# Performance work log

Hardware: AMD Instinct MI355X
Metric: run time of the kernel (lower is better)

## Reference

```python
import jax, jax.numpy as jnp
import numpy as np

B, T, D, HS = 8, 2048, 768, 64
H = D // HS  # 12 heads
LN_EPS = 1e-5


def setup_inputs() -> dict:
    key = jax.random.key(0)
    ks = jax.random.split(key, 8)
    s = 0.02
    x = jax.random.normal(ks[0], (B, T, D), jnp.float32)
    Wx = jax.random.normal(ks[1], (D, D), jnp.float32) * s
    Ww = jax.random.normal(ks[2], (D, D), jnp.float32) * 0.01  # w_proj.weight ~ N(0,0.01)
    # w_proj bias schedule: logit(1 - linspace(0.9,0.999,H)) per head, expanded over head_size
    r_sched = jnp.linspace(0.9, 0.999, H)
    w_target = 1.0 - r_sched
    bw = jnp.log(w_target / (1.0 - w_target))          # logit
    bw = jnp.repeat(bw[:, None], HS, axis=1).reshape(-1)  # (D,)
    Wk = jax.random.normal(ks[3], (D, D), jnp.float32) * s
    Wv = jax.random.normal(ks[4], (D, D), jnp.float32) * s
    Wr = jax.random.normal(ks[5], (D, D), jnp.float32) * s
    Wo = jax.random.normal(ks[6], (D, D), jnp.float32) * s
    gamma = jnp.ones((D,), jnp.float32)
    beta = jnp.zeros((D,), jnp.float32)
    return {"x": x, "Wx": Wx, "Ww": Ww, "bw": bw, "Wk": Wk, "Wv": Wv,
            "Wr": Wr, "Wo": Wo, "gamma": gamma, "beta": beta}


def _layernorm(x, gamma, beta):
    mu = jnp.mean(x, axis=-1, keepdims=True)
    var = jnp.mean(jnp.square(x - mu), axis=-1, keepdims=True)
    return (x - mu) * jax.lax.rsqrt(var + LN_EPS) * gamma + beta


def _selective_scan(k, v, w):
    """k,v,w: (T,B,H,HS). State S: (B,H,HS,HS).
    S_t = (1 - w_t) * S_{t-1} (decay along key dim) + k_t (x) v_t;  y_t = k_t . S_t."""
    S0 = jnp.zeros((B, H, HS, HS), k.dtype)

    def step(S, inp):
        kt, vt, wt = inp  # each (B,H,HS)
        S = S * (1.0 - wt)[..., :, None] + kt[..., :, None] * vt[..., None, :]
        yt = jnp.einsum('bhi,bhij->bhj', kt, S)
        return S, yt

    _, ys = jax.lax.scan(step, S0, (k, v, w))
    return ys  # (T,B,H,HS)


def reference(x, Wx, Ww, bw, Wk, Wv, Wr, Wo, gamma, beta):
    xn = _layernorm(x, gamma, beta)                       # (B,T,D)
    xp = jnp.einsum('btd,ed->bte', xn, Wx)                # x_proj
    w = jax.nn.sigmoid(jnp.einsum('bte,fe->btf', xp, Ww) + bw)
    k = jnp.einsum('btd,ed->bte', xn, Wk)
    v = jnp.einsum('btd,ed->bte', xn, Wv)
    r = jax.nn.sigmoid(jnp.einsum('btd,ed->bte', xn, Wr))

    def to_scan(a):  # (B,T,D) -> (T,B,H,HS)
        return a.reshape(B, T, H, HS).transpose(1, 0, 2, 3)

    ys = _selective_scan(to_scan(k), to_scan(v), to_scan(w))  # (T,B,H,HS)
    y = ys.transpose(1, 0, 2, 3).reshape(B, T, D)
    y = y * r
    return jnp.einsum('btd,ed->bte', y, Wo)
```

## Files before the change

kernel.cpp:

```cpp
#include <hip/hip_runtime.h>

#define B_ 8
#define T_ 2048
#define D_ 768
#define H_ 12
#define HS_ 64
#define LN_EPS 1e-5f
#define NC 32
#define TC 64

typedef __attribute__((ext_vector_type(8))) short bf16x8;
typedef __attribute__((ext_vector_type(4))) float f32x4;

__device__ __forceinline__ ushort f2bf(float f) {
  unsigned u = __builtin_bit_cast(unsigned, f);
  unsigned r = (u + 0x7FFFu + ((u >> 16) & 1u)) >> 16;
  return (ushort)r;
}
__device__ __forceinline__ float bf2f(ushort u) {
  return __builtin_bit_cast(float, ((unsigned)u) << 16);
}

__device__ __forceinline__ int fragaddr(int t, int i) {
  return ((t >> 4) * 2 + (i >> 5)) * 512 + ((((i >> 3) & 3) * 16) + (t & 15)) * 8 + (i & 7);
}
__device__ __forceinline__ int fragswz(int i) {
  return (((i >> 3) & 3) << 3) ^ (((i >> 5) & 1) << 5);
}

__global__ __launch_bounds__(256) void zero_out_kernel(float* __restrict__ out, int n) {
  for (int i = blockIdx.x * 256 + threadIdx.x; i < n; i += gridDim.x * 256)
    out[i] = 0.f;
}

__global__ __launch_bounds__(256) void cast5_kernel(
    const float* __restrict__ w0, const float* __restrict__ w1,
    const float* __restrict__ w2, const float* __restrict__ w3,
    const float* __restrict__ w4, ushort* __restrict__ dst) {
  const float* srcs[5] = {w0, w1, w2, w3, w4};
  const int slots[5] = {0, 1, 2, 4, 5};
  const float* src = srcs[blockIdx.y];
  ushort* d = dst + (size_t)slots[blockIdx.y] * 589824;
  int idx = (blockIdx.x * 256 + threadIdx.x) * 4;
  float4 v = *reinterpret_cast<const float4*>(src + idx);
  ushort4 o;
  o.x = f2bf(v.x); o.y = f2bf(v.y); o.z = f2bf(v.z); o.w = f2bf(v.w);
  *reinterpret_cast<ushort4*>(d + idx) = o;
}

__global__ __launch_bounds__(256) void transpose_cast_kernel(
    const float* __restrict__ src, ushort* __restrict__ dst) {
  __shared__ ushort tile[32][33];
  const int bx = blockIdx.x * 32;
  const int by = blockIdx.y * 32;
  const int tx = threadIdx.x & 31, ty = threadIdx.x >> 5;
#pragma unroll
  for (int r = 0; r < 32; r += 8)
    tile[ty + r][tx] = f2bf(src[(size_t)(by + ty + r) * 768 + bx + tx]);
  __syncthreads();
#pragma unroll
  for (int r = 0; r < 32; r += 8)
    dst[(size_t)(bx + ty + r) * 768 + by + tx] = tile[tx][ty + r];
}

__global__ __launch_bounds__(256) void ln_kernel(
    const float* __restrict__ x, const float* __restrict__ gamma,
    const float* __restrict__ beta, ushort* __restrict__ xn) {
  const int wv = threadIdx.x >> 6;
  const int lane = threadIdx.x & 63;
  const int row = blockIdx.x * 4 + wv;
  const float* xr = x + (size_t)row * D_;
  float4 a[3];
#pragma unroll
  for (int s = 0; s < 3; ++s)
    a[s] = *reinterpret_cast<const float4*>(xr + s * 256 + lane * 4);
  float sum = 0.f;
#pragma unroll
  for (int s = 0; s < 3; ++s) sum += a[s].x + a[s].y + a[s].z + a[s].w;
#pragma unroll
  for (int off = 32; off; off >>= 1) sum += __shfl_xor(sum, off);
  float mu = sum * (1.f / 768.f);
  float vs = 0.f;
#pragma unroll
  for (int s = 0; s < 3; ++s) {
    float dx = a[s].x - mu, dy = a[s].y - mu, dz = a[s].z - mu, dw = a[s].w - mu;
    vs += dx * dx + dy * dy + dz * dz + dw * dw;
  }
#pragma unroll
  for (int off = 32; off; off >>= 1) vs += __shfl_xor(vs, off);
  float rs = rsqrtf(vs * (1.f / 768.f) + LN_EPS);
  ushort* orow = xn + (size_t)row * D_;
#pragma unroll
  for (int s = 0; s < 3; ++s) {
    int col = s * 256 + lane * 4;
    float4 g = *reinterpret_cast<const float4*>(gamma + col);
    float4 bb = *reinterpret_cast<const float4*>(beta + col);
    ushort4 o;
    o.x = f2bf((a[s].x - mu) * rs * g.x + bb.x);
    o.y = f2bf((a[s].y - mu) * rs * g.y + bb.y);
    o.z = f2bf((a[s].z - mu) * rs * g.z + bb.z);
    o.w = f2bf((a[s].w - mu) * rs * g.w + bb.w);
    *reinterpret_cast<ushort4*>(orow + col) = o;
  }
}

__global__ __launch_bounds__(512, 2) void gemm256(
    const ushort* __restrict__ A, const ushort* __restrict__ W,
    float* __restrict__ Cf,
    ushort* __restrict__ d0, ushort* __restrict__ d1,
    ushort* __restrict__ d2, ushort* __restrict__ d3, int mode) {
  __shared__ __align__(16) ushort lds[65536];
  const int tid = threadIdx.x;
  const int wid = tid >> 6;
  const int lane = tid & 63;
  const int wr = wid >> 2, wc = wid & 3;
  const int fr = lane & 15, fq = lane >> 4;
  const int m0 = blockIdx.x * 256, n0 = blockIdx.y * 256;
  const int strow = tid >> 3;
  const int stblk = tid & 7;

  const int RA0 = wr * 8192;
  const int RA1 = 32768 + wr * 8192;
  const int RB0 = 16384 + (wc >> 1) * 8192 + (wc & 1) * 4096;
  const int RB1 = 49152 + (wc >> 1) * 8192 + (wc & 1) * 4096;

  f32x4 acc[8][4];
#pragma unroll
  for (int m = 0; m < 8; ++m)
#pragma unroll
    for (int n = 0; n < 4; ++n) acc[m][n] = (f32x4){0.f, 0.f, 0.f, 0.f};

#define STAGE_HALF(gb, grow0, kk0, roff)                                          \
  {                                                                               \
    _Pragma("unroll") for (int j = 0; j < 2; ++j) {                               \
      const int lr_ = j * 64 + strow;                                             \
      const int bs_ = stblk ^ (lr_ & 7);                                          \
      const ushort* s_ = (gb) + (size_t)((grow0) + lr_) * 768 + (kk0) + bs_ * 8;  \
      __builtin_amdgcn_global_load_lds(                                           \
          (const __attribute__((address_space(1))) void*)s_,                      \
          (__attribute__((address_space(3))) void*)(lds + (roff) + j * 4096 + wid * 512), \
          16, 0, 0);                                                              \
    }                                                                             \
  }

#define LDF(dst, base, rf, kk)                                                    \
  dst = *reinterpret_cast<const bf16x8*>(                                         \
      lds + (base) + ((rf)*16 + fr) * 64 + ((((kk)*4 + fq) ^ (fr & 7)) * 8));

#define MFMA_Q(mb, nb, aa, bb)                                                    \
  __builtin_amdgcn_s_setprio(1);                                                  \
  _Pragma("unroll") for (int m_ = 0; m_ < 4; ++m_)                                \
  _Pragma("unroll") for (int n_ = 0; n_ < 2; ++n_)                                \
  _Pragma("unroll") for (int k_ = 0; k_ < 2; ++k_)                                \
    acc[(mb) + m_][(nb) + n_] = __builtin_amdgcn_mfma_f32_16x16x32_bf16(          \
        aa[m_][k_], bb[n_][k_], acc[(mb) + m_][(nb) + n_], 0, 0, 0);              \
  __builtin_amdgcn_s_setprio(0);

  STAGE_HALF(A, m0, 0, 0);
  STAGE_HALF(A, m0 + 128, 0, 8192);
  STAGE_HALF(W, n0, 0, 16384);
  STAGE_HALF(W, n0 + 128, 0, 24576);
  STAGE_HALF(W, n0, 64, 49152);
  STAGE_HALF(W, n0 + 128, 64, 57344);
  asm volatile("s_waitcnt vmcnt(4)" ::: "memory");
  __builtin_amdgcn_s_barrier();

  bf16x8 aL[4][2], aH[4][2], bL[2][2], bH[2][2];

  for (int i = 0; i < 6; ++i) {
    const int kQ = (2 * i + 1) * 64;
    const int kP2 = (2 * i + 2 <= 11 ? 2 * i + 2 : 11) * 64;
    const int kQ2 = (2 * i + 3 <= 11 ? 2 * i + 3 : 11) * 64;

    STAGE_HALF(A, m0, kQ, 32768);
#pragma unroll
    for (int m = 0; m < 4; ++m) { LDF(aL[m][0], RA0, m, 0); LDF(aL[m][1], RA0, m, 1); }
#pragma unroll
    for (int n = 0; n < 2; ++n) { LDF(bL[n][0], RB0, n, 0); LDF(bL[n][1], RB0, n, 1); }
    __builtin_amdgcn_s_barrier();
    MFMA_Q(0, 0, aL, bL);
    __builtin_amdgcn_s_barrier();

    STAGE_HALF(A, m0 + 128, kQ, 40960);
#pragma unroll
    for (int n = 0; n < 2; ++n) { LDF(bH[n][0], RB0, n + 2, 0); LDF(bH[n][1], RB0, n + 2, 1); }
    __builtin_amdgcn_s_barrier();
    MFMA_Q(0, 2, aL, bH);
    __builtin_amdgcn_s_barrier();

    STAGE_HALF(W, n0, kP2, 16384);
#pragma unroll
    for (int m = 0; m < 4; ++m) { LDF(aH[m][0], RA0, m + 4, 0); LDF(aH[m][1], RA0, m + 4, 1); }
    __builtin_amdgcn_s_barrier();
    MFMA_Q(4, 0, aH, bL);
    __builtin_amdgcn_s_barrier();

    STAGE_HALF(W, n0 + 128, kP2, 24576);
    __builtin_amdgcn_s_barrier();
    MFMA_Q(4, 2, aH, bH);
    asm volatile("s_waitcnt vmcnt(4)" ::: "memory");
    __builtin_amdgcn_s_barrier();

    STAGE_HALF(A, m0, kP2, 0);
#pragma unroll
    for (int m = 0; m < 4; ++m) { LDF(aL[m][0], RA1, m, 0); LDF(aL[m][1], RA1, m, 1); }
#pragma unroll
    for (int n = 0; n < 2; ++n) { LDF(bL[n][0], RB1, n, 0); LDF(bL[n][1], RB1, n, 1); }
    __builtin_amdgcn_s_barrier();
    MFMA_Q(0, 0, aL, bL);
    __builtin_amdgcn_s_barrier();

    STAGE_HALF(A, m0 + 128, kP2, 8192);
#pragma unroll
    for (int n = 0; n < 2; ++n) { LDF(bH[n][0], RB1, n + 2, 0); LDF(bH[n][1], RB1, n + 2, 1); }
    __builtin_amdgcn_s_barrier();
    MFMA_Q(0, 2, aL, bH);
    __builtin_amdgcn_s_barrier();

    STAGE_HALF(W, n0, kQ2, 49152);
#pragma unroll
    for (int m = 0; m < 4; ++m) { LDF(aH[m][0], RA1, m + 4, 0); LDF(aH[m][1], RA1, m + 4, 1); }
    __builtin_amdgcn_s_barrier();
    MFMA_Q(4, 0, aH, bL);
    __builtin_amdgcn_s_barrier();

    STAGE_HALF(W, n0 + 128, kQ2, 57344);
    __builtin_amdgcn_s_barrier();
    MFMA_Q(4, 2, aH, bH);
    asm volatile("s_waitcnt vmcnt(4)" ::: "memory");
    __builtin_amdgcn_s_barrier();
  }

  const int r0 = fq * 4;
  if (mode == 5) {
    const int sel = n0 >= 2304 ? 3 : n0 >= 1536 ? 2 : n0 >= 768 ? 1 : 0;
    const int nb = n0 - sel * 768;
    if (sel == 1) {
#pragma unroll
      for (int mf = 0; mf < 8; ++mf)
#pragma unroll
        for (int nf = 0; nf < 4; ++nf) {
          int gr = m0 + wr * 128 + mf * 16 + r0;
          int gc = nb + wc * 64 + nf * 16 + fr;
          int b = gr >> 11, t = gr & 2047;
          int c = t >> 6, s0 = t & 63;
          int h = gc >> 6, j = gc & 63;
          size_t addr = ((size_t)((b * 12 + h) * 32 + c)) * 4096 +
                        (size_t)(((j >> 4) * 2 + (s0 >> 5)) * 512 +
                                 (((s0 >> 3) & 3) * 16 + (j & 15)) * 8 + (s0 & 7));
          ushort4 o;
          o.x = f2bf(acc[mf][nf][0]); o.y = f2bf(acc[mf][nf][1]);
          o.z = f2bf(acc[mf][nf][2]); o.w = f2bf(acc[mf][nf][3]);
          *reinterpret_cast<ushort4*>(d1 + addr) = o;
        }
    } else {
      ushort* dst = sel == 0 ? d0 : sel == 2 ? d2 : d3;
      const bool sig = (sel == 2);
#pragma unroll
      for (int mf = 0; mf < 8; ++mf)
#pragma unroll
        for (int nf = 0; nf < 4; ++nf) {
          int gr = m0 + wr * 128 + mf * 16 + r0;
          int gc = nb + wc * 64 + nf * 16 + fr;
#pragma unroll
          for (int rr = 0; rr < 4; ++rr) {
            float v = acc[mf][nf][rr];
            if (sig) v = 1.f / (1.f + __expf(-v));
            dst[(size_t)(gr + rr) * 768 + gc] = f2bf(v);
          }
        }
    }
  } else {
#pragma unroll
    for (int mf = 0; mf < 8; ++mf)
#pragma unroll
      for (int nf = 0; nf < 4; ++nf) {
        int gr = m0 + wr * 128 + mf * 16 + r0;
        int gc = n0 + wc * 64 + nf * 16 + fr;
#pragma unroll
        for (int rr = 0; rr < 4; ++rr)
          Cf[(size_t)(gr + rr) * 768 + gc] = acc[mf][nf][rr];
      }
  }
#undef STAGE_HALF
#undef LDF
#undef MFMA_Q
}

__global__ __launch_bounds__(256) void scan_mc3(
    const ushort* __restrict__ kb, const ushort* __restrict__ zb,
    const ushort* __restrict__ vbF, const float* __restrict__ bwp,
    ushort* __restrict__ McT, float* __restrict__ aend) {
  __shared__ ushort kt[64 * 72];
  __shared__ ushort zt[64 * 72];
  __shared__ ushort kIAfA[4096];
  __shared__ float part[256];
  const int bh = blockIdx.x, c = blockIdx.y;
  const int b = bh / H_, h = bh % H_;
  const int tid = threadIdx.x;
  const int w = tid >> 6, lane = tid & 63;
  const int fr = lane & 15, fq = lane >> 4;
  const int row = tid >> 2, c16 = (tid & 3) * 16;
  const float bwh = bwp[h * 64];

  {
    const ushort* gk = kb + ((size_t)(b * T_ + c * TC + row)) * 768 + h * 64 + c16;
    const ushort* gz = zb + ((size_t)(b * T_ + c * TC + row)) * 768 + h * 64 + c16;
    uint4 k0 = *(const uint4*)gk, k1 = *(const uint4*)(gk + 8);
    uint4 z0 = *(const uint4*)gz, z1 = *(const uint4*)(gz + 8);
    *reinterpret_cast<uint4*>(&kt[row * 72 + c16]) = k0;
    *reinterpret_cast<uint4*>(&kt[row * 72 + c16 + 8]) = k1;
    *reinterpret_cast<uint4*>(&zt[row * 72 + c16]) = z0;
    *reinterpret_cast<uint4*>(&zt[row * 72 + c16 + 8]) = z1;
  }
  bf16x8 vfr[8];
  {
    const ushort* vch = vbF + ((size_t)bh * NC + c) * 4096;
#pragma unroll
    for (int f = 0; f < 8; ++f)
      vfr[f] = *reinterpret_cast<const bf16x8*>(vch + f * 512 + lane * 8);
  }
  __syncthreads();
  float dreg[16];
  float p = 1.f;
#pragma unroll
  for (int tt = 0; tt < 16; ++tt) {
    float z = bf2f(zt[(w * 16 + tt) * 72 + lane]);
    float d = 1.f / (1.f + __expf(z + bwh));
    dreg[tt] = d;
    p *= d;
  }
  part[w * 64 + lane] = p;
  __syncthreads();
  float a = 1.f;
  for (int w2 = 0; w2 < w; ++w2) a *= part[w2 * 64 + lane];
  if (w == 0)
    aend[((size_t)bh * NC + c) * 64 + lane] =
        part[lane] * part[64 + lane] * part[128 + lane] * part[192 + lane];
#pragma unroll
  for (int tt = 0; tt < 16; ++tt) {
    int t = w * 16 + tt;
    float k = bf2f(kt[t * 72 + lane]);
    a *= dreg[tt];
    kIAfA[fragaddr(lane, t)] = f2bf(k / a);
  }
  __syncthreads();

  bf16x8 af2[2];
#pragma unroll
  for (int kk = 0; kk < 2; ++kk)
    af2[kk] = *reinterpret_cast<const bf16x8*>(&kIAfA[(w * 2 + kk) * 512 + lane * 8]);
  f32x4 accM[4];
#pragma unroll
  for (int nf = 0; nf < 4; ++nf) accM[nf] = (f32x4){0.f, 0.f, 0.f, 0.f};
#pragma unroll
  for (int kk = 0; kk < 2; ++kk)
#pragma unroll
    for (int nf = 0; nf < 4; ++nf)
      accM[nf] = __builtin_amdgcn_mfma_f32_16x16x32_bf16(af2[kk], vfr[nf * 2 + kk], accM[nf], 0, 0, 0);
  ushort* mch = McT + ((size_t)bh * NC + c) * 4096;
#pragma unroll
  for (int nf = 0; nf < 4; ++nf) {
    ushort4 o;
    o.x = f2bf(accM[nf][0]); o.y = f2bf(accM[nf][1]);
    o.z = f2bf(accM[nf][2]); o.w = f2bf(accM[nf][3]);
    *reinterpret_cast<ushort4*>(&mch[(nf * 16 + fr) * 64 + w * 16 + fq * 4]) = o;
  }
}

__global__ __launch_bounds__(256) void scan_chain3(
    const ushort* __restrict__ McT, const float* __restrict__ aend,
    ushort* __restrict__ S0F) {
  const int bh = blockIdx.x;
  const int j = threadIdx.x >> 2, i0 = (threadIdx.x & 3) * 16;
  const int fbase = ((j >> 4) * 2 + (i0 >> 5)) * 512 + (((i0 >> 3) & 3) * 16 + (j & 15)) * 8;
  float S[16];
#pragma unroll
  for (int p = 0; p < 16; ++p) S[p] = 0.f;

  const ushort* mch0 = McT + ((size_t)bh * NC) * 4096 + j * 64 + i0;
  const float* aep0 = aend + ((size_t)bh * NC) * 64 + i0;
  bf16x8 m0 = *reinterpret_cast<const bf16x8*>(mch0);
  bf16x8 m1 = *reinterpret_cast<const bf16x8*>(mch0 + 8);
  float4 a0 = *(const float4*)(aep0);
  float4 a1 = *(const float4*)(aep0 + 4);
  float4 a2 = *(const float4*)(aep0 + 8);
  float4 a3 = *(const float4*)(aep0 + 12);

  for (int c = 0; c < NC; ++c) {
    int cn = c + 1 < NC ? c + 1 : NC - 1;
    const ushort* mchn = McT + ((size_t)bh * NC + cn) * 4096 + j * 64 + i0;
    const float* aepn = aend + ((size_t)bh * NC + cn) * 64 + i0;
    bf16x8 n0 = *reinterpret_cast<const bf16x8*>(mchn);
    bf16x8 n1 = *reinterpret_cast<const bf16x8*>(mchn + 8);
    float4 b0 = *(const float4*)(aepn);
    float4 b1 = *(const float4*)(aepn + 4);
    float4 b2 = *(const float4*)(aepn + 8);
    float4 b3 = *(const float4*)(aepn + 12);

    ushort* s0 = S0F + ((size_t)bh * NC + c) * 4096 + fbase;
    ushort4 o0, o1, o2, o3;
    o0.x = f2bf(S[0]); o0.y = f2bf(S[1]); o0.z = f2bf(S[2]); o0.w = f2bf(S[3]);
    o1.x = f2bf(S[4]); o1.y = f2bf(S[5]); o1.z = f2bf(S[6]); o1.w = f2bf(S[7]);
    o2.x = f2bf(S[8]); o2.y = f2bf(S[9]); o2.z = f2bf(S[10]); o2.w = f2bf(S[11]);
    o3.x = f2bf(S[12]); o3.y = f2bf(S[13]); o3.z = f2bf(S[14]); o3.w = f2bf(S[15]);
    *reinterpret_cast<ushort4*>(s0) = o0;
    *reinterpret_cast<ushort4*>(s0 + 4) = o1;
    *reinterpret_cast<ushort4*>(s0 + 128) = o2;
    *reinterpret_cast<ushort4*>(s0 + 132) = o3;

    float av[16];
    av[0] = a0.x; av[1] = a0.y; av[2] = a0.z; av[3] = a0.w;
    av[4] = a1.x; av[5] = a1.y; av[6] = a1.z; av[7] = a1.w;
    av[8] = a2.x; av[9] = a2.y; av[10] = a2.z; av[11] = a2.w;
    av[12] = a3.x; av[13] = a3.y; av[14] = a3.z; av[15] = a3.w;
#pragma unroll
    for (int p = 0; p < 8; ++p) S[p] = av[p] * (S[p] + bf2f((ushort)m0[p]));
#pragma unroll
    for (int p = 0; p < 8; ++p) S[8 + p] = av[8 + p] * (S[8 + p] + bf2f((ushort)m1[p]));

    m0 = n0; m1 = n1; a0 = b0; a1 = b1; a2 = b2; a3 = b3;
  }
}

__global__ __launch_bounds__(256, 1) void scan_y3(
    const ushort* __restrict__ kb, const ushort* __restrict__ zb,
    const ushort* __restrict__ vbF, const ushort* __restrict__ rb,
    const ushort* __restrict__ S0F, const float* __restrict__ bwp,
    ushort* __restrict__ yrow) {
  __shared__ ushort kt[64 * 72];
  __shared__ ushort zt[64 * 72];
  __shared__ ushort kAf[4096];
  __shared__ ushort kIAfB[4096];
  __shared__ ushort Am[64 * 72];
  __shared__ float part[256];
  const int bh = blockIdx.x, c = blockIdx.y;
  const int b = bh / H_, h = bh % H_;
  const int tid = threadIdx.x;
  const int w = tid >> 6, lane = tid & 63;
  const int fr = lane & 15, fq = lane >> 4;
  const int row = tid >> 2, c16 = (tid & 3) * 16;
  const float bwh = bwp[h * 64];
  const int swz = fragswz(lane);

  {
    const ushort* gk = kb + ((size_t)(b * T_ + c * TC + row)) * 768 + h * 64 + c16;
    const ushort* gz = zb + ((size_t)(b * T_ + c * TC + row)) * 768 + h * 64 + c16;
    uint4 k0 = *(const uint4*)gk, k1 = *(const uint4*)(gk + 8);
    uint4 z0 = *(const uint4*)gz, z1 = *(const uint4*)(gz + 8);
    *reinterpret_cast<uint4*>(&kt[row * 72 + c16]) = k0;
    *reinterpret_cast<uint4*>(&kt[row * 72 + c16 + 8]) = k1;
    *reinterpret_cast<uint4*>(&zt[row * 72 + c16]) = z0;
    *reinterpret_cast<uint4*>(&zt[row * 72 + c16 + 8]) = z1;
  }
  bf16x8 vfr[8];
  {
    const ushort* vch = vbF + ((size_t)bh * NC + c) * 4096;
#pragma unroll
    for (int f = 0; f < 8; ++f)
      vfr[f] = *reinterpret_cast<const bf16x8*>(vch + f * 512 + lane * 8);
  }
  ushort rr[16];
  {
    const ushort* rrow = rb + ((size_t)(b * T_ + c * TC)) * 768 + h * 64;
#pragma unroll
    for (int tp = 0; tp < 4; ++tp)
#pragma unroll
      for (int nf = 0; nf < 4; ++nf)
        rr[tp * 4 + nf] = rrow[(size_t)(w * 16 + fq * 4 + tp) * 768 + nf * 16 + fr];
  }
  __syncthreads();
  float dreg[16];
  float p = 1.f;
#pragma unroll
  for (int tt = 0; tt < 16; ++tt) {
    float z = bf2f(zt[(w * 16 + tt) * 72 + lane]);
    float d = 1.f / (1.f + __expf(z + bwh));
    dreg[tt] = d;
    p *= d;
  }
  part[w * 64 + lane] = p;
  __syncthreads();
  float a = 1.f;
  for (int w2 = 0; w2 < w; ++w2) a *= part[w2 * 64 + lane];
#pragma unroll
  for (int tt = 0; tt < 16; ++tt) {
    int t = w * 16 + tt;
    float k = bf2f(kt[t * 72 + lane]);
    a *= dreg[tt];
    int ad = fragaddr(t, lane) ^ swz;
    kAf[ad] = f2bf(k * a);
    kIAfB[ad] = f2bf(k / a);
  }
  __syncthreads();

  bf16x8 af[2];
#pragma unroll
  for (int kk = 0; kk < 2; ++kk) {
    int ra = ((w * 2 + kk) * 512 + lane * 8) ^ (((lane >> 4) << 3) ^ (kk << 5));
    af[kk] = *reinterpret_cast<const bf16x8*>(&kAf[ra]);
  }
  {
    f32x4 accA[4];
#pragma unroll
    for (int nf = 0; nf < 4; ++nf) accA[nf] = (f32x4){0.f, 0.f, 0.f, 0.f};
#pragma unroll
    for (int kk = 0; kk < 2; ++kk)
#pragma unroll
      for (int nf = 0; nf < 4; ++nf) {
        int rb8 = ((nf * 2 + kk) * 512 + lane * 8) ^ (((lane >> 4) << 3) ^ (kk << 5));
        bf16x8 b8 = *reinterpret_cast<const bf16x8*>(&kIAfB[rb8]);
        accA[nf] = __builtin_amdgcn_mfma_f32_16x16x32_bf16(af[kk], b8, accA[nf], 0, 0, 0);
      }
#pragma unroll
    for (int nf = 0; nf < 4; ++nf)
#pragma unroll
      for (int q = 0; q < 4; ++q) {
        int t = w * 16 + fq * 4 + q;
        int s = nf * 16 + fr;
        Am[t * 72 + s] = f2bf((s <= t) ? accA[nf][q] : 0.f);
      }
  }
  __syncthreads();

  f32x4 accY[4];
#pragma unroll
  for (int nf = 0; nf < 4; ++nf) accY[nf] = (f32x4){0.f, 0.f, 0.f, 0.f};
  const ushort* s0ch = S0F + ((size_t)bh * NC + c) * 4096;
#pragma unroll
  for (int kk = 0; kk < 2; ++kk)
#pragma unroll
    for (int nf = 0; nf < 4; ++nf) {
      bf16x8 b8 = *reinterpret_cast<const bf16x8*>(s0ch + (nf * 2 + kk) * 512 + lane * 8);
      accY[nf] = __builtin_amdgcn_mfma_f32_16x16x32_bf16(af[kk], b8, accY[nf], 0, 0, 0);
    }
#pragma unroll
  for (int kk = 0; kk < 2; ++kk) {
    bf16x8 am8 = *reinterpret_cast<const bf16x8*>(&Am[(w * 16 + fr) * 72 + kk * 32 + fq * 8]);
#pragma unroll
    for (int nf = 0; nf < 4; ++nf)
      accY[nf] = __builtin_amdgcn_mfma_f32_16x16x32_bf16(am8, vfr[nf * 2 + kk], accY[nf], 0, 0, 0);
  }
#pragma unroll
  for (int nf = 0; nf < 4; ++nf)
#pragma unroll
    for (int q = 0; q < 4; ++q) {
      int t = w * 16 + fq * 4 + q;
      int j = nf * 16 + fr;
      size_t go = ((size_t)(b * T_ + c * TC + t)) * 768 + h * 64 + j;
      yrow[go] = f2bf(accY[nf][q] * bf2f(rr[q * 4 + nf]));
    }
}

extern "C" void kernel_launch(void* const* d_in, const int* in_sizes, int n_in,
                              void* d_out, int out_size, void* d_ws, size_t ws_size,
                              hipStream_t stream) {
  const float* x     = (const float*)d_in[0];
  const float* Wx    = (const float*)d_in[1];
  const float* Ww    = (const float*)d_in[2];
  const float* bw    = (const float*)d_in[3];
  const float* Wk    = (const float*)d_in[4];
  const float* Wv    = (const float*)d_in[5];
  const float* Wr    = (const float*)d_in[6];
  const float* Wo    = (const float*)d_in[7];
  const float* gamma = (const float*)d_in[8];
  const float* beta  = (const float*)d_in[9];
  float* out = (float*)d_out;

  const size_t NEED = 208404480ull;
  if (ws_size < NEED) {
    zero_out_kernel<<<2048, 256, 0, stream>>>(out, out_size);
    return;
  }

  char* ws = (char*)d_ws;
  ushort* xn  = (ushort*)ws;
  ushort* wb  = (ushort*)(ws + 25165824);
  ushort* WxT = (ushort*)(ws + 32243712);
  ushort* kb  = (ushort*)(ws + 57409536);
  ushort* vbF = (ushort*)(ws + 82575360);
  ushort* rb  = (ushort*)(ws + 107741184);
  ushort* yr  = (ushort*)(ws + 132907008);
  ushort* zb  = (ushort*)(ws + 158072832);
  ushort* McT = (ushort*)ws;
  ushort* S0F = (ushort*)(ws + 32243712);
  float*  aendb = (float*)(ws + 132907008);

  ushort* WcatB = wb;
  ushort* Mb  = wb + 3 * 589824;
  ushort* WoB = wb + 4 * 589824;
  ushort* WwB = wb + 5 * 589824;

  cast5_kernel<<<dim3(576, 5), 256, 0, stream>>>(Wk, Wv, Wr, Wo, Ww, wb);
  transpose_cast_kernel<<<dim3(24, 24), 256, 0, stream>>>(Wx, WxT);
  gemm256<<<dim3(3, 3), 512, 0, stream>>>(WwB, WxT, nullptr, Mb, nullptr, nullptr,
                                          nullptr, 5);
  ln_kernel<<<4096, 256, 0, stream>>>(x, gamma, beta, xn);

  gemm256<<<dim3(64, 12), 512, 0, stream>>>(xn, WcatB, nullptr, kb, vbF, rb, zb, 5);

  scan_mc3<<<dim3(96, NC), 256, 0, stream>>>(kb, zb, vbF, bw, McT, aendb);
  scan_chain3<<<96, 256, 0, stream>>>(McT, aendb, S0F);
  scan_y3<<<dim3(96, NC), 256, 0, stream>>>(kb, zb, vbF, rb, S0F, bw, yr);

  gemm256<<<dim3(64, 3), 512, 0, stream>>>(yr, WoB, out, nullptr, nullptr, nullptr,
                                           nullptr, 0);
}
```

Before: 241.7 us.

## Merge GEMM sub-phases into two per half-step and fuse weight prep kernels

The gemm256 main loop now issues both A (or both W) half-stages and all fragment loads up front, then runs two MFMA quarters back-to-back under raised priority. This halves the number of barriers per k-step, at the cost of more registers held live and less interleaving of loads with compute. Separately, the weight cast and the Wx transpose-cast are fused into one prep_kernel launch to save a kernel launch.

```diff
diff --git a/kernel.cpp b/kernel.cpp
--- a/kernel.cpp
+++ b/kernel.cpp
@@ -33,34 +33,34 @@
     out[i] = 0.f;
 }
 
-__global__ __launch_bounds__(256) void cast5_kernel(
+__global__ __launch_bounds__(256) void prep_kernel(
     const float* __restrict__ w0, const float* __restrict__ w1,
     const float* __restrict__ w2, const float* __restrict__ w3,
-    const float* __restrict__ w4, ushort* __restrict__ dst) {
-  const float* srcs[5] = {w0, w1, w2, w3, w4};
-  const int slots[5] = {0, 1, 2, 4, 5};
-  const float* src = srcs[blockIdx.y];
-  ushort* d = dst + (size_t)slots[blockIdx.y] * 589824;
-  int idx = (blockIdx.x * 256 + threadIdx.x) * 4;
-  float4 v = *reinterpret_cast<const float4*>(src + idx);
-  ushort4 o;
-  o.x = f2bf(v.x); o.y = f2bf(v.y); o.z = f2bf(v.z); o.w = f2bf(v.w);
-  *reinterpret_cast<ushort4*>(d + idx) = o;
-}
-
-__global__ __launch_bounds__(256) void transpose_cast_kernel(
-    const float* __restrict__ src, ushort* __restrict__ dst) {
-  __shared__ ushort tile[32][33];
-  const int bx = blockIdx.x * 32;
-  const int by = blockIdx.y * 32;
-  const int tx = threadIdx.x & 31, ty = threadIdx.x >> 5;
-#pragma unroll
-  for (int r = 0; r < 32; r += 8)
-    tile[ty + r][tx] = f2bf(src[(size_t)(by + ty + r) * 768 + bx + tx]);
-  __syncthreads();
-#pragma unroll
-  for (int r = 0; r < 32; r += 8)
-    dst[(size_t)(bx + ty + r) * 768 + by + tx] = tile[tx][ty + r];
+    const float* __restrict__ w4, const float* __restrict__ Wx,
+    ushort* __restrict__ dst, ushort* __restrict__ WxT) {
+  if (blockIdx.y < 5) {
+    const float* srcs[5] = {w0, w1, w2, w3, w4};
+    const int slots[5] = {0, 1, 2, 4, 5};
+    const float* src = srcs[blockIdx.y];
+    ushort* d = dst + (size_t)slots[blockIdx.y] * 589824;
+    int idx = (blockIdx.x * 256 + threadIdx.x) * 4;
+    float4 v = *reinterpret_cast<const float4*>(src + idx);
+    ushort4 o;
+    o.x = f2bf(v.x); o.y = f2bf(v.y); o.z = f2bf(v.z); o.w = f2bf(v.w);
+    *reinterpret_cast<ushort4*>(d + idx) = o;
+  } else {
+    __shared__ ushort tile[32][33];
+    const int bx = (blockIdx.x % 24) * 32;
+    const int by = (blockIdx.x / 24) * 32;
+    const int tx = threadIdx.x & 31, ty = threadIdx.x >> 5;
+#pragma unroll
+    for (int r = 0; r < 32; r += 8)
+      tile[ty + r][tx] = f2bf(Wx[(size_t)(by + ty + r) * 768 + bx + tx]);
+    __syncthreads();
+#pragma unroll
+    for (int r = 0; r < 32; r += 8)
+      WxT[(size_t)(bx + ty + r) * 768 + by + tx] = tile[tx][ty + r];
+  }
 }
 
 __global__ __launch_bounds__(256) void ln_kernel(
@@ -148,13 +148,20 @@
       lds + (base) + ((rf)*16 + fr) * 64 + ((((kk)*4 + fq) ^ (fr & 7)) * 8));
 
 #define MFMA_Q(mb, nb, aa, bb)                                                    \
-  __builtin_amdgcn_s_setprio(1);                                                  \
   _Pragma("unroll") for (int m_ = 0; m_ < 4; ++m_)                                \
   _Pragma("unroll") for (int n_ = 0; n_ < 2; ++n_)                                \
   _Pragma("unroll") for (int k_ = 0; k_ < 2; ++k_)                                \
     acc[(mb) + m_][(nb) + n_] = __builtin_amdgcn_mfma_f32_16x16x32_bf16(          \
-        aa[m_][k_], bb[n_][k_], acc[(mb) + m_][(nb) + n_], 0, 0, 0);              \
-  __builtin_amdgcn_s_setprio(0);
+        aa[m_][k_], bb[n_][k_], acc[(mb) + m_][(nb) + n_], 0, 0, 0);
+
+#define LDF_AL(RA) \
+  _Pragma("unroll") for (int m = 0; m < 4; ++m) { LDF(aL[m][0], RA, m, 0); LDF(aL[m][1], RA, m, 1); }
+#define LDF_AH(RA) \
+  _Pragma("unroll") for (int m = 0; m < 4; ++m) { LDF(aH[m][0], RA, m + 4, 0); LDF(aH[m][1], RA, m + 4, 1); }
+#define LDF_BL(RB) \
+  _Pragma("unroll") for (int n = 0; n < 2; ++n) { LDF(bL[n][0], RB, n, 0); LDF(bL[n][1], RB, n, 1); }
+#define LDF_BH(RB) \
+  _Pragma("unroll") for (int n = 0; n < 2; ++n) { LDF(bH[n][0], RB, n + 2, 0); LDF(bH[n][1], RB, n + 2, 1); }
 
   STAGE_HALF(A, m0, 0, 0);
   STAGE_HALF(A, m0 + 128, 0, 8192);
@@ -173,60 +180,46 @@
     const int kQ2 = (2 * i + 3 <= 11 ? 2 * i + 3 : 11) * 64;
 
     STAGE_HALF(A, m0, kQ, 32768);
-#pragma unroll
-    for (int m = 0; m < 4; ++m) { LDF(aL[m][0], RA0, m, 0); LDF(aL[m][1], RA0, m, 1); }
-#pragma unroll
-    for (int n = 0; n < 2; ++n) { LDF(bL[n][0], RB0, n, 0); LDF(bL[n][1], RB0, n, 1); }
-    __builtin_amdgcn_s_barrier();
+    STAGE_HALF(A, m0 + 128, kQ, 40960);
+    LDF_AL(RA0);
+    LDF_BL(RB0);
+    LDF_BH(RB0);
+    __builtin_amdgcn_s_barrier();
+    __builtin_amdgcn_s_setprio(1);
     MFMA_Q(0, 0, aL, bL);
-    __builtin_amdgcn_s_barrier();
-
-    STAGE_HALF(A, m0 + 128, kQ, 40960);
-#pragma unroll
-    for (int n = 0; n < 2; ++n) { LDF(bH[n][0], RB0, n + 2, 0); LDF(bH[n][1], RB0, n + 2, 1); }
-    __builtin_amdgcn_s_barrier();
     MFMA_Q(0, 2, aL, bH);
-    __builtin_amdgcn_s_barrier();
-
+    __builtin_amdgcn_s_setprio(0);
+    __builtin_amdgcn_s_barrier();
     STAGE_HALF(W, n0, kP2, 16384);
-#pragma unroll
-    for (int m = 0; m < 4; ++m) { LDF(aH[m][0], RA0, m + 4, 0); LDF(aH[m][1], RA0, m + 4, 1); }
-    __builtin_amdgcn_s_barrier();
+    STAGE_HALF(W, n0 + 128, kP2, 24576);
+    LDF_AH(RA0);
+    __builtin_amdgcn_s_barrier();
+    __builtin_amdgcn_s_setprio(1);
     MFMA_Q(4, 0, aH, bL);
-    __builtin_amdgcn_s_barrier();
-
-    STAGE_HALF(W, n0 + 128, kP2, 24576);
-    __builtin_amdgcn_s_barrier();
     MFMA_Q(4, 2, aH, bH);
+    __builtin_amdgcn_s_setprio(0);
     asm volatile("s_waitcnt vmcnt(4)" ::: "memory");
     __builtin_amdgcn_s_barrier();
 
     STAGE_HALF(A, m0, kP2, 0);
-#pragma unroll
-    for (int m = 0; m < 4; ++m) { LDF(aL[m][0], RA1, m, 0); LDF(aL[m][1], RA1, m, 1); }
-#pragma unroll
-    for (int n = 0; n < 2; ++n) { LDF(bL[n][0], RB1, n, 0); LDF(bL[n][1], RB1, n, 1); }
-    __builtin_amdgcn_s_barrier();
+    STAGE_HALF(A, m0 + 128, kP2, 8192);
+    LDF_AL(RA1);
+    LDF_BL(RB1);
+    LDF_BH(RB1);
+    __builtin_amdgcn_s_barrier();
+    __builtin_amdgcn_s_setprio(1);
     MFMA_Q(0, 0, aL, bL);
-    __builtin_amdgcn_s_barrier();
-
-    STAGE_HALF(A, m0 + 128, kP2, 8192);
-#pragma unroll
-    for (int n = 0; n < 2; ++n) { LDF(bH[n][0], RB1, n + 2, 0); LDF(bH[n][1], RB1, n + 2, 1); }
-    __builtin_amdgcn_s_barrier();
     MFMA_Q(0, 2, aL, bH);
-    __builtin_amdgcn_s_barrier();
-
+    __builtin_amdgcn_s_setprio(0);
+    __builtin_amdgcn_s_barrier();
     STAGE_HALF(W, n0, kQ2, 49152);
-#pragma unroll
-    for (int m = 0; m < 4; ++m) { LDF(aH[m][0], RA1, m + 4, 0); LDF(aH[m][1], RA1, m + 4, 1); }
-    __builtin_amdgcn_s_barrier();
+    STAGE_HALF(W, n0 + 128, kQ2, 57344);
+    LDF_AH(RA1);
+    __builtin_amdgcn_s_barrier();
+    __builtin_amdgcn_s_setprio(1);
     MFMA_Q(4, 0, aH, bL);
-    __builtin_amdgcn_s_barrier();
-
-    STAGE_HALF(W, n0 + 128, kQ2, 57344);
-    __builtin_amdgcn_s_barrier();
     MFMA_Q(4, 2, aH, bH);
+    __builtin_amdgcn_s_setprio(0);
     asm volatile("s_waitcnt vmcnt(4)" ::: "memory");
     __builtin_amdgcn_s_barrier();
   }
@@ -285,6 +278,10 @@
 #undef STAGE_HALF
 #undef LDF
 #undef MFMA_Q
+#undef LDF_AL
+#undef LDF_AH
+#undef LDF_BL
+#undef LDF_BH
 }
 
 __global__ __launch_bounds__(256) void scan_mc3(
@@ -591,8 +588,7 @@
   ushort* WoB = wb + 4 * 589824;
   ushort* WwB = wb + 5 * 589824;
 
-  cast5_kernel<<<dim3(576, 5), 256, 0, stream>>>(Wk, Wv, Wr, Wo, Ww, wb);
-  transpose_cast_kernel<<<dim3(24, 24), 256, 0, stream>>>(Wx, WxT);
+  prep_kernel<<<dim3(576, 6), 256, 0, stream>>>(Wk, Wv, Wr, Wo, Ww, Wx, wb, WxT);
   gemm256<<<dim3(3, 3), 512, 0, stream>>>(WwB, WxT, nullptr, Mb, nullptr, nullptr,
                                           nullptr, 5);
   ln_kernel<<<4096, 256, 0, stream>>>(x, gamma, beta, xn);
```

Result: no change. 238.7 us (-1.2%).
